# Kernel optimization log

Measured on AMD Instinct MI355X. Metric: run time of the kernel, lower is better.

Reference implementation:

```python
import jax, jax.numpy as jnp
import numpy as np
from math import pi

FC_IN, FC_OUT = 64, 64
LABEL_NC = 35
B, C, H, W = 2, 64, 128, 128
EPS = 1e-5
SLOPE = 0.01  # torch leaky_relu default


def _pa(h, w):
    # absolute normalized coordinates, matches init_pos buffers
    xs = (jnp.arange(h, dtype=jnp.float32) / h) * 2.0 - 1.0
    ys = (jnp.arange(w, dtype=jnp.float32) / w) * 2.0 - 1.0
    px = jnp.broadcast_to(xs[:, None], (h, w))
    py = jnp.broadcast_to(ys[None, :], (h, w))
    return jnp.stack([px, py], 0)  # (2,h,w)


def _coords(h, w):
    # f0=3; while-loop runs once (f=3 -> f=1), so exactly 4 channels
    f = 3.0
    ang_x = 2.0 * pi * jnp.remainder(jnp.arange(w, dtype=jnp.float32), f) / f
    ang_y = 2.0 * pi * jnp.remainder(jnp.arange(h, dtype=jnp.float32), f) / f
    xcos = jnp.broadcast_to(jnp.cos(ang_x)[None, :], (h, w))
    xsin = jnp.broadcast_to(jnp.sin(ang_x)[None, :], (h, w))
    ycos = jnp.broadcast_to(jnp.cos(ang_y)[:, None], (h, w))
    ysin = jnp.broadcast_to(jnp.sin(ang_y)[:, None], (h, w))
    return jnp.stack([xcos, xsin, ycos, ysin], 0)  # (4,h,w)


def _nearest(t, h, w):
    # F.interpolate(mode='nearest') index map: floor(i*in/out)
    ih = jnp.arange(h) * t.shape[2] // h
    iw = jnp.arange(w) * t.shape[3] // w
    return t[:, :, ih][:, :, :, iw]


def setup_inputs() -> dict:
    key = jax.random.key(0)
    ks = jax.random.split(key, 7)
    return {
        "x": jax.random.normal(ks[0], (B, C, H, W), jnp.float32),
        "layout": jax.random.normal(ks[1], (B, LABEL_NC, H, W), jnp.float32),
        "pr": jax.random.normal(ks[2], (B, 2, H, W), jnp.float32),
        "conv_w": jax.random.normal(ks[3], (1, 10), jnp.float32) * 0.02,
        "conv_b": jnp.zeros((1,), jnp.float32),
        "W_table": jax.random.normal(ks[4], (LABEL_NC, FC_IN * FC_OUT), jnp.float32),
        "b_table": jax.random.normal(ks[5], (LABEL_NC, FC_OUT), jnp.float32) * 0.02,
        "pl": jax.random.normal(ks[6], (2, H, W), jnp.float32),
    }


def reference(x, layout, pr, conv_w, conv_b, W_table, b_table, pl):
    b, c, h, w = x.shape
    pa = jnp.broadcast_to(_pa(h, w)[None], (b, 2, h, w))
    plb = jnp.broadcast_to(pl[None], (b, 2, h, w))
    coords = jnp.broadcast_to(_coords(h, w)[None], (b, 4, h, w))
    prr = _nearest(pr, h, w)
    pos = jnp.concatenate([pa, plb, prr, coords], axis=1)  # (B,10,h,w)
    # 1x1 conv to a single channel, broadcast-added over C
    x = x + jnp.einsum('bchw,oc->bohw', pos, conv_w) + conv_b[None, :, None, None]
    # argmax-routed per-pixel affine params
    lay = _nearest(layout, h, w)
    arg = jnp.argmax(lay, axis=1)  # (B,h,w) int
    Wg = W_table[arg].reshape(b, h, w, FC_IN, FC_OUT)  # huge gathered tensor (as in original)
    bg = b_table[arg]  # (B,h,w,FC_OUT)
    xh = jnp.transpose(x, (0, 2, 3, 1))  # (B,h,w,C)
    y = jnp.einsum('bhwc,bhwco->bhwo', xh, Wg) + bg
    y = jnp.transpose(y, (0, 3, 1, 2))  # (B,FC_OUT,h,w)
    # instance norm (no affine, biased variance, eps=1e-5)
    mu = jnp.mean(y, axis=(2, 3), keepdims=True)
    var = jnp.var(y, axis=(2, 3), keepdims=True)
    y = (y - mu) * jax.lax.rsqrt(var + EPS)
    return jnp.where(y >= 0, y, SLOPE * y)
```

## Files before the change

kernel.cpp:

```cpp
#include <hip/hip_runtime.h>

#define HH 128
#define WW 128
#define CC 64
#define OO 64
#define NC 35
#define NPIX (HH*WW)
#define LISTST NPIX
#define NBKT (2*NC)
#define XSTR 68


__global__ __launch_bounds__(256) void prep_kernel(
    const float* __restrict__ x, const float* __restrict__ layout,
    const float* __restrict__ pr, const float* __restrict__ cw,
    const float* __restrict__ cb, const float* __restrict__ pl,
    float* __restrict__ xT, int* __restrict__ lab)
{
    __shared__ float s_xh[64*33];
    __shared__ float s_s[32];

    const int t    = threadIdx.x;
    const int wv   = t >> 6;
    const int lane = t & 63;
    const int tile = blockIdx.x;
    const int b    = tile >> 9;
    const int rem  = tile & 511;
    const int h    = rem >> 2;
    const int w0   = (rem & 3) << 5;

    if (wv == 0 && lane < 32) {
        int w = w0 + lane;
        float pxv = (float)h * (2.0f/128.0f) - 1.0f;
        float pyv = (float)w * (2.0f/128.0f) - 1.0f;
        float pl0 = pl[h*WW + w];
        float pl1 = pl[NPIX + h*WW + w];
        float pr0 = pr[((b*2+0)*HH + h)*WW + w];
        float pr1 = pr[((b*2+1)*HH + h)*WW + w];
        int kx = w % 3, kyy = h % 3;
        const float C1 = -0.5f, S1 = 0.86602540378443864676f;
        float xcv = (kx==0)  ? 1.0f : C1;
        float xsv = (kx==0)  ? 0.0f : ((kx==1)  ? S1 : -S1);
        float ycv = (kyy==0) ? 1.0f : C1;
        float ysv = (kyy==0) ? 0.0f : ((kyy==1) ? S1 : -S1);
        s_s[lane] = cb[0] + pxv*cw[0] + pyv*cw[1] + pl0*cw[2] + pl1*cw[3]
                  + pr0*cw[4] + pr1*cw[5] + xcv*cw[6] + xsv*cw[7]
                  + ycv*cw[8] + ysv*cw[9];
    }

    if (wv == 1 && lane < 32) {
        int w = w0 + lane;
        const float* lp = layout + ((size_t)(b*NC)*HH + h)*WW + w;
        float best = lp[0]; int bi = 0;
        #pragma unroll
        for (int c = 1; c < NC; ++c) {
            float v = lp[(size_t)c*NPIX];
            if (v > best) { best = v; bi = c; }
        }
        lab[b*NPIX + h*WW + w] = bi;
    }

    {
        int p = t & 31, c0 = t >> 5;
        const float* xp = x + ((size_t)(b*CC)*HH + h)*WW + w0 + p;
        #pragma unroll
        for (int k = 0; k < 8; ++k) {
            int c = c0 + 8*k;
            s_xh[c*33 + p] = xp[(size_t)c*NPIX];
        }
    }
    __syncthreads();

    {
        int p = t >> 3, c0 = (t & 7) << 3;
        float sp = s_s[p];
        float4 a, d;
        a.x = s_xh[(c0+0)*33+p] + sp;
        a.y = s_xh[(c0+1)*33+p] + sp;
        a.z = s_xh[(c0+2)*33+p] + sp;
        a.w = s_xh[(c0+3)*33+p] + sp;
        d.x = s_xh[(c0+4)*33+p] + sp;
        d.y = s_xh[(c0+5)*33+p] + sp;
        d.z = s_xh[(c0+6)*33+p] + sp;
        d.w = s_xh[(c0+7)*33+p] + sp;
        float* dst = xT + (((size_t)b*NPIX + h*WW + w0 + p) << 6) + c0;
        *(float4*)dst       = a;
        *(float4*)(dst + 4) = d;
    }
}

__global__ __launch_bounds__(256) void bin_kernel(
    const int* __restrict__ lab, int* __restrict__ cnt, int* __restrict__ list)
{
    __shared__ int s_wsum[4];
    const int t    = threadIdx.x;
    const int lane = t & 63;
    const int wv   = t >> 6;
    const int bkt  = blockIdx.x;
    const int b    = (bkt >= NC) ? 1 : 0;
    const int l    = bkt - b*NC;
    const int* lp  = lab + b*NPIX;

    int m = 0;
    #pragma unroll 8
    for (int j = 0; j < 64; ++j) m += (lp[j*256 + t] == l) ? 1 : 0;

    int v = m;
    #pragma unroll
    for (int d = 1; d < 64; d <<= 1) {
        int o = __shfl_up(v, d);
        if (lane >= d) v += o;
    }
    if (lane == 63) s_wsum[wv] = v;
    __syncthreads();
    int wbase = 0;
    #pragma unroll
    for (int k = 0; k < 4; ++k) wbase += (k < wv) ? s_wsum[k] : 0;
    int base = wbase + v - m;
    if (t == 0) cnt[bkt] = s_wsum[0] + s_wsum[1] + s_wsum[2] + s_wsum[3];

    int* dst = list + bkt*LISTST;
    int o = base;
    #pragma unroll 8
    for (int j = 0; j < 64; ++j) {
        int p = j*256 + t;
        if (lp[p] == l) dst[o++] = p;
    }
}

#define FMA_PX(A, XV) \
    A.x = fmaf((XV), qv.x, A.x); \
    A.y = fmaf((XV), qv.y, A.y); \
    A.z = fmaf((XV), qv.z, A.z); \
    A.w = fmaf((XV), qv.w, A.w);

__global__ __launch_bounds__(256) void mv_kernel(
    const float* __restrict__ Wt, const float* __restrict__ bt,
    const float* __restrict__ xT, const int* __restrict__ cnt,
    const int* __restrict__ list, float* __restrict__ yT,
    float* __restrict__ gpad)
{
    __shared__ __align__(16) float s_xh[64*XSTR];
    __shared__ int   s_pib[64];
    __shared__ float s_red[4][64][2];
    __shared__ int   s_ntask;

    const int t    = threadIdx.x;
    const int wv   = t >> 6;
    const int lane = t & 63;
    const int i15  = lane & 15;
    const int ihi  = lane >> 4;

    if (t < 64) {
        int c1 = cnt[(lane < NBKT) ? lane : (NBKT-1)];
        int c2 = cnt[(lane < (NBKT-64)) ? 64 + lane : (NBKT-1)];
        int m  = c1 > c2 ? c1 : c2;
        #pragma unroll
        for (int d = 32; d >= 1; d >>= 1) {
            int o = __shfl_xor(m, d);
            m = m > o ? m : o;
        }
        if (lane == 0) s_ntask = NBKT * ((m + 63) >> 6);
    }
    __syncthreads();
    const int ntask = s_ntask;

    for (int task = blockIdx.x; task < ntask; task += gridDim.x) {
        const int bkt   = task % NBKT;
        const int chunk = task / NBKT;
        const int n     = cnt[bkt];
        const int base  = chunk << 6;
        if (base >= n) continue;
        const int b = (bkt >= NC) ? 1 : 0;
        const int l = bkt - b*NC;

        __syncthreads();

        {
            const int p   = t & 63;
            const int q   = t >> 6;
            const int pi  = base + p;
            const int pib = list[bkt*LISTST + ((pi < n) ? pi : (n-1))];
            if (q == 0) s_pib[p] = pib;
            const float* xp = xT + (((size_t)b*NPIX + pib) << 6) + (q << 4);
            #pragma unroll
            for (int j = 0; j < 4; ++j) {
                float4 v = ((const float4*)xp)[j];
                const int c = (q << 4) + (j << 2);
                s_xh[(c+0)*XSTR + p] = v.x;
                s_xh[(c+1)*XSTR + p] = v.y;
                s_xh[(c+2)*XSTR + p] = v.z;
                s_xh[(c+3)*XSTR + p] = v.w;
            }
        }
        __syncthreads();

        const float4* __restrict__ W4 = ((const float4*)(Wt + (size_t)l*4096)) + lane;
        const float4 bb = *((const float4*)(bt + (size_t)l*64) + i15);
        float4 sumv = make_float4(0,0,0,0), ssv = make_float4(0,0,0,0);

        #pragma unroll
        for (int g = 0; g < 2; ++g) {
            const int p0 = (wv << 4) + (g << 3);
            float4 a[8];
            #pragma unroll
            for (int pj = 0; pj < 8; ++pj) a[pj] = make_float4(0,0,0,0);

            #pragma unroll
            for (int tt = 0; tt < 16; ++tt) {
                const float4 qv = W4[tt << 6];
                const int    c  = (tt << 2) + ihi;
                const float4 xa = *(const float4*)&s_xh[c*XSTR + p0];
                const float4 xb = *(const float4*)&s_xh[c*XSTR + p0 + 4];
                FMA_PX(a[0], xa.x) FMA_PX(a[1], xa.y) FMA_PX(a[2], xa.z) FMA_PX(a[3], xa.w)
                FMA_PX(a[4], xb.x) FMA_PX(a[5], xb.y) FMA_PX(a[6], xb.z) FMA_PX(a[7], xb.w)
            }

            #pragma unroll
            for (int pj = 0; pj < 8; ++pj) {
                a[pj].x += __shfl_xor(a[pj].x, 16); a[pj].y += __shfl_xor(a[pj].y, 16);
                a[pj].z += __shfl_xor(a[pj].z, 16); a[pj].w += __shfl_xor(a[pj].w, 16);
                a[pj].x += __shfl_xor(a[pj].x, 32); a[pj].y += __shfl_xor(a[pj].y, 32);
                a[pj].z += __shfl_xor(a[pj].z, 32); a[pj].w += __shfl_xor(a[pj].w, 32);
            }

            if (ihi == 0) {
                #pragma unroll
                for (int pj = 0; pj < 8; ++pj) {
                    const bool  vld = (base + p0 + pj) < n;
                    const float msk = vld ? 1.0f : 0.0f;
                    float y0 = (a[pj].x + bb.x) * msk;
                    float y1 = (a[pj].y + bb.y) * msk;
                    float y2 = (a[pj].z + bb.z) * msk;
                    float y3 = (a[pj].w + bb.w) * msk;
                    if (vld) {
                        float* yp = yT + (((size_t)b*NPIX + s_pib[p0+pj]) << 6) + (i15 << 2);
                        *(float4*)yp = make_float4(y0, y1, y2, y3);
                    }
                    sumv.x += y0; ssv.x += y0*y0;
                    sumv.y += y1; ssv.y += y1*y1;
                    sumv.z += y2; ssv.z += y2*y2;
                    sumv.w += y3; ssv.w += y3*y3;
                }
            }
        }

        if (ihi == 0) {
            const int o = i15 << 2;
            s_red[wv][o+0][0] = sumv.x; s_red[wv][o+0][1] = ssv.x;
            s_red[wv][o+1][0] = sumv.y; s_red[wv][o+1][1] = ssv.y;
            s_red[wv][o+2][0] = sumv.z; s_red[wv][o+2][1] = ssv.z;
            s_red[wv][o+3][0] = sumv.w; s_red[wv][o+3][1] = ssv.w;
        }
        __syncthreads();
        if (t < 64) {
            float S  = s_red[0][t][0] + s_red[1][t][0] + s_red[2][t][0] + s_red[3][t][0];
            float SS = s_red[0][t][1] + s_red[1][t][1] + s_red[2][t][1] + s_red[3][t][1];
            float* gp = gpad + (((b << 6) + t) << 4);
            atomicAdd(gp + 0, S);
            atomicAdd(gp + 1, SS);
        }
    }
}

__global__ __launch_bounds__(256) void norm_kernel(
    const float* __restrict__ yT, const float* __restrict__ gpad,
    float* __restrict__ out)
{
    __shared__ float s_t[64*65];
    __shared__ float s_mean[64];
    __shared__ float s_rstd[64];

    const int t    = threadIdx.x;
    const int tile = blockIdx.x;
    const int b    = tile >> 8;
    const int rem  = tile & 255;
    const int h    = rem >> 1;
    const int w0   = (rem & 1) << 6;

    if (t < 64) {
        const float invN = 1.0f/16384.0f;
        const float* gp = gpad + (((b << 6) + t) << 4);
        float mean = gp[0] * invN;
        float var  = gp[1] * invN - mean*mean;
        s_mean[t] = mean;
        s_rstd[t] = rsqrtf(var + 1e-5f);
    }
    {
        const int p = t >> 2, q = t & 3;
        const float4* yp = (const float4*)(yT + (((size_t)b*NPIX + h*WW + w0 + p) << 6) + (q << 4));
        #pragma unroll
        for (int j = 0; j < 4; ++j) {
            float4 v = yp[j];
            int o = (q << 4) + (j << 2);
            s_t[(o+0)*65 + p] = v.x;
            s_t[(o+1)*65 + p] = v.y;
            s_t[(o+2)*65 + p] = v.z;
            s_t[(o+3)*65 + p] = v.w;
        }
    }
    __syncthreads();
    {
        const int o = t >> 2, q = t & 3;
        const float mean = s_mean[o];
        const float r    = s_rstd[o];
        float* op = out + (((size_t)(b*OO + o)*HH + h)*WW) + w0 + (q << 4);
        #pragma unroll
        for (int j = 0; j < 4; ++j) {
            int wq = (q << 4) + (j << 2);
            float4 v;
            v.x = s_t[o*65 + wq + 0];
            v.y = s_t[o*65 + wq + 1];
            v.z = s_t[o*65 + wq + 2];
            v.w = s_t[o*65 + wq + 3];
            float a_;
            a_ = (v.x - mean) * r; v.x = (a_ >= 0.f) ? a_ : 0.01f*a_;
            a_ = (v.y - mean) * r; v.y = (a_ >= 0.f) ? a_ : 0.01f*a_;
            a_ = (v.z - mean) * r; v.z = (a_ >= 0.f) ? a_ : 0.01f*a_;
            a_ = (v.w - mean) * r; v.w = (a_ >= 0.f) ? a_ : 0.01f*a_;
            ((float4*)op)[j] = v;
        }
    }
}

extern "C" void kernel_launch(void* const* d_in, const int* in_sizes, int n_in,
                              void* d_out, int out_size, void* d_ws, size_t ws_size,
                              hipStream_t stream) {
    const float* x      = (const float*)d_in[0];
    const float* layout = (const float*)d_in[1];
    const float* pr     = (const float*)d_in[2];
    const float* cw     = (const float*)d_in[3];
    const float* cb     = (const float*)d_in[4];
    const float* Wt     = (const float*)d_in[5];
    const float* bt     = (const float*)d_in[6];
    const float* pl     = (const float*)d_in[7];
    float* out = (float*)d_out;

    char*  ws   = (char*)d_ws;
    float* gpad = (float*)ws;
    int*   cnt  = (int*)(ws + 8192);
    int*   lab  = (int*)(ws + 16384);
    int*   list = (int*)(ws + (256u << 10));
    float* xT   = (float*)(ws + (8u  << 20));
    float* yT   = (float*)(ws + (16u << 20));

    hipMemsetAsync(gpad, 0, 8192, stream);
    prep_kernel<<<1024, 256, 0, stream>>>(x, layout, pr, cw, cb, pl, xT, lab);
    bin_kernel <<<  70, 256, 0, stream>>>(lab, cnt, list);
    mv_kernel  <<<1024, 256, 0, stream>>>(Wt, bt, xT, cnt, list, yT, gpad);
    norm_kernel<<< 512, 256, 0, stream>>>(yT, gpad, out);
}
```

Baseline: 128.1 us.

## Fuse all four stages into one cooperative persistent kernel with grid syncs

Replaces the memset plus four separate launches with a single cooperative kernel of 512 blocks that runs prep, binning, the routed matvec and the normalisation phases, separated by grid-wide syncs. Shared memory is unioned across phases, and the gpad zeroing moves into the binning phase. The aim is to remove launch gaps and kernel boundaries. In exchange, grid syncs are costly, each block does two prep tiles serially, and the binning phase runs on only 70 blocks while the rest wait. If the cooperative launch fails, the original multi-kernel path still runs.

```diff
diff --git a/kernel.cpp b/kernel.cpp
--- a/kernel.cpp
+++ b/kernel.cpp
@@ -1,4 +1,7 @@
 #include <hip/hip_runtime.h>
+#include <hip/hip_cooperative_groups.h>
+
+namespace cg = cooperative_groups;
 
 #define HH 128
 #define WW 128
@@ -9,6 +12,311 @@
 #define LISTST NPIX
 #define NBKT (2*NC)
 #define XSTR 68
+#define GRID 512
+
+
+#define FMA_PX(A, XV) \
+    A.x = fmaf((XV), qv.x, A.x); \
+    A.y = fmaf((XV), qv.y, A.y); \
+    A.z = fmaf((XV), qv.z, A.z); \
+    A.w = fmaf((XV), qv.w, A.w);
+
+__global__ void __launch_bounds__(256, 2) fused_kernel(
+    const float* __restrict__ x, const float* __restrict__ layout,
+    const float* __restrict__ pr, const float* __restrict__ cw,
+    const float* __restrict__ cb, const float* __restrict__ Wt,
+    const float* __restrict__ bt, const float* __restrict__ pl,
+    float* __restrict__ out, float* __restrict__ gpad, int* __restrict__ cnt,
+    int* __restrict__ lab, int* __restrict__ list,
+    float* __restrict__ xT, float* __restrict__ yT)
+{
+    __shared__ __align__(16) union {
+        struct { float xh[64*33]; float s[32]; } prep;
+        struct { int wsum[4]; } bin;
+        struct { float xh[64*XSTR]; float red[4][64][2]; int pib[64]; int ntask; } mv;
+        struct { float tmat[64*65]; float mean[64]; float rstd[64]; } norm;
+    } u;
+
+    cg::grid_group gg = cg::this_grid();
+
+    const int t    = threadIdx.x;
+    const int bid  = blockIdx.x;
+    const int wv   = t >> 6;
+    const int lane = t & 63;
+    const int i15  = lane & 15;
+    const int ihi  = lane >> 4;
+
+    for (int tile = bid; tile < 1024; tile += GRID) {
+        const int b  = tile >> 9;
+        const int rem = tile & 511;
+        const int h  = rem >> 2;
+        const int w0 = (rem & 3) << 5;
+
+        if (wv == 0 && lane < 32) {
+            int w = w0 + lane;
+            float pxv = (float)h * (2.0f/128.0f) - 1.0f;
+            float pyv = (float)w * (2.0f/128.0f) - 1.0f;
+            float pl0 = pl[h*WW + w];
+            float pl1 = pl[NPIX + h*WW + w];
+            float pr0 = pr[((b*2+0)*HH + h)*WW + w];
+            float pr1 = pr[((b*2+1)*HH + h)*WW + w];
+            int kx = w % 3, kyy = h % 3;
+            const float C1 = -0.5f, S1 = 0.86602540378443864676f;
+            float xcv = (kx==0)  ? 1.0f : C1;
+            float xsv = (kx==0)  ? 0.0f : ((kx==1)  ? S1 : -S1);
+            float ycv = (kyy==0) ? 1.0f : C1;
+            float ysv = (kyy==0) ? 0.0f : ((kyy==1) ? S1 : -S1);
+            u.prep.s[lane] = cb[0] + pxv*cw[0] + pyv*cw[1] + pl0*cw[2] + pl1*cw[3]
+                      + pr0*cw[4] + pr1*cw[5] + xcv*cw[6] + xsv*cw[7]
+                      + ycv*cw[8] + ysv*cw[9];
+        }
+
+        if (wv == 1 && lane < 32) {
+            int w = w0 + lane;
+            const float* lp = layout + ((size_t)(b*NC)*HH + h)*WW + w;
+            float best = lp[0]; int bi = 0;
+            #pragma unroll
+            for (int c = 1; c < NC; ++c) {
+                float v = lp[(size_t)c*NPIX];
+                if (v > best) { best = v; bi = c; }
+            }
+            lab[b*NPIX + h*WW + w] = bi;
+        }
+
+        {
+            int p = t & 31, c0 = t >> 5;
+            const float* xp = x + ((size_t)(b*CC)*HH + h)*WW + w0 + p;
+            #pragma unroll
+            for (int k = 0; k < 8; ++k) {
+                int c = c0 + 8*k;
+                u.prep.xh[c*33 + p] = xp[(size_t)c*NPIX];
+            }
+        }
+        __syncthreads();
+
+        {
+            int p = t >> 3, c0 = (t & 7) << 3;
+            float sp = u.prep.s[p];
+            float4 a, d;
+            a.x = u.prep.xh[(c0+0)*33+p] + sp;
+            a.y = u.prep.xh[(c0+1)*33+p] + sp;
+            a.z = u.prep.xh[(c0+2)*33+p] + sp;
+            a.w = u.prep.xh[(c0+3)*33+p] + sp;
+            d.x = u.prep.xh[(c0+4)*33+p] + sp;
+            d.y = u.prep.xh[(c0+5)*33+p] + sp;
+            d.z = u.prep.xh[(c0+6)*33+p] + sp;
+            d.w = u.prep.xh[(c0+7)*33+p] + sp;
+            float* dst = xT + (((size_t)b*NPIX + h*WW + w0 + p) << 6) + c0;
+            *(float4*)dst       = a;
+            *(float4*)(dst + 4) = d;
+        }
+        __syncthreads();
+    }
+
+    gg.sync();
+
+    if (bid < NBKT) {
+        const int bkt = bid;
+        const int b   = (bkt >= NC) ? 1 : 0;
+        const int l   = bkt - b*NC;
+        const int* lp = lab + b*NPIX;
+
+        int m = 0;
+        #pragma unroll 8
+        for (int j = 0; j < 64; ++j) m += (lp[j*256 + t] == l) ? 1 : 0;
+
+        int v = m;
+        #pragma unroll
+        for (int d = 1; d < 64; d <<= 1) {
+            int o = __shfl_up(v, d);
+            if (lane >= d) v += o;
+        }
+        if (lane == 63) u.bin.wsum[wv] = v;
+        __syncthreads();
+        int wbase = 0;
+        #pragma unroll
+        for (int k = 0; k < 4; ++k) wbase += (k < wv) ? u.bin.wsum[k] : 0;
+        int base = wbase + v - m;
+        if (t == 0) cnt[bkt] = u.bin.wsum[0] + u.bin.wsum[1] + u.bin.wsum[2] + u.bin.wsum[3];
+
+        int* dst = list + bkt*LISTST;
+        int o = base;
+        #pragma unroll 8
+        for (int j = 0; j < 64; ++j) {
+            int p = j*256 + t;
+            if (lp[p] == l) dst[o++] = p;
+        }
+    } else if (bid == NBKT) {
+        for (int i = t; i < 2048; i += 256) gpad[i] = 0.0f;
+    }
+
+    gg.sync();
+
+    if (t < 64) {
+        int c1 = cnt[(lane < NBKT) ? lane : (NBKT-1)];
+        int c2 = cnt[(lane < (NBKT-64)) ? 64 + lane : (NBKT-1)];
+        int m  = c1 > c2 ? c1 : c2;
+        #pragma unroll
+        for (int d = 32; d >= 1; d >>= 1) {
+            int o = __shfl_xor(m, d);
+            m = m > o ? m : o;
+        }
+        if (lane == 0) u.mv.ntask = NBKT * ((m + 63) >> 6);
+    }
+    __syncthreads();
+    const int ntask = u.mv.ntask;
+
+    for (int task = bid; task < ntask; task += GRID) {
+        const int bkt   = task % NBKT;
+        const int chunk = task / NBKT;
+        const int n     = cnt[bkt];
+        const int base  = chunk << 6;
+        if (base >= n) continue;
+        const int b = (bkt >= NC) ? 1 : 0;
+        const int l = bkt - b*NC;
+
+        __syncthreads();
+
+        {
+            const int p   = t & 63;
+            const int q   = t >> 6;
+            const int pi  = base + p;
+            const int pib = list[bkt*LISTST + ((pi < n) ? pi : (n-1))];
+            if (q == 0) u.mv.pib[p] = pib;
+            const float* xp = xT + (((size_t)b*NPIX + pib) << 6) + (q << 4);
+            #pragma unroll
+            for (int j = 0; j < 4; ++j) {
+                float4 v = ((const float4*)xp)[j];
+                const int c = (q << 4) + (j << 2);
+                u.mv.xh[(c+0)*XSTR + p] = v.x;
+                u.mv.xh[(c+1)*XSTR + p] = v.y;
+                u.mv.xh[(c+2)*XSTR + p] = v.z;
+                u.mv.xh[(c+3)*XSTR + p] = v.w;
+            }
+        }
+        __syncthreads();
+
+        const float4* __restrict__ W4 = ((const float4*)(Wt + (size_t)l*4096)) + lane;
+        const float4 bb = *((const float4*)(bt + (size_t)l*64) + i15);
+        float4 sumv = make_float4(0,0,0,0), ssv = make_float4(0,0,0,0);
+
+        #pragma unroll
+        for (int g = 0; g < 2; ++g) {
+            const int p0 = (wv << 4) + (g << 3);
+            float4 a[8];
+            #pragma unroll
+            for (int pj = 0; pj < 8; ++pj) a[pj] = make_float4(0,0,0,0);
+
+            #pragma unroll
+            for (int tt = 0; tt < 16; ++tt) {
+                const float4 qv = W4[tt << 6];
+                const int    c  = (tt << 2) + ihi;
+                const float4 xa = *(const float4*)&u.mv.xh[c*XSTR + p0];
+                const float4 xb = *(const float4*)&u.mv.xh[c*XSTR + p0 + 4];
+                FMA_PX(a[0], xa.x) FMA_PX(a[1], xa.y) FMA_PX(a[2], xa.z) FMA_PX(a[3], xa.w)
+                FMA_PX(a[4], xb.x) FMA_PX(a[5], xb.y) FMA_PX(a[6], xb.z) FMA_PX(a[7], xb.w)
+            }
+
+            #pragma unroll
+            for (int pj = 0; pj < 8; ++pj) {
+                a[pj].x += __shfl_xor(a[pj].x, 16); a[pj].y += __shfl_xor(a[pj].y, 16);
+                a[pj].z += __shfl_xor(a[pj].z, 16); a[pj].w += __shfl_xor(a[pj].w, 16);
+                a[pj].x += __shfl_xor(a[pj].x, 32); a[pj].y += __shfl_xor(a[pj].y, 32);
+                a[pj].z += __shfl_xor(a[pj].z, 32); a[pj].w += __shfl_xor(a[pj].w, 32);
+            }
+
+            if (ihi == 0) {
+                #pragma unroll
+                for (int pj = 0; pj < 8; ++pj) {
+                    const bool  vld = (base + p0 + pj) < n;
+                    const float msk = vld ? 1.0f : 0.0f;
+                    float y0 = (a[pj].x + bb.x) * msk;
+                    float y1 = (a[pj].y + bb.y) * msk;
+                    float y2 = (a[pj].z + bb.z) * msk;
+                    float y3 = (a[pj].w + bb.w) * msk;
+                    if (vld) {
+                        float* yp = yT + (((size_t)b*NPIX + u.mv.pib[p0+pj]) << 6) + (i15 << 2);
+                        *(float4*)yp = make_float4(y0, y1, y2, y3);
+                    }
+                    sumv.x += y0; ssv.x += y0*y0;
+                    sumv.y += y1; ssv.y += y1*y1;
+                    sumv.z += y2; ssv.z += y2*y2;
+                    sumv.w += y3; ssv.w += y3*y3;
+                }
+            }
+        }
+
+        if (ihi == 0) {
+            const int o = i15 << 2;
+            u.mv.red[wv][o+0][0] = sumv.x; u.mv.red[wv][o+0][1] = ssv.x;
+            u.mv.red[wv][o+1][0] = sumv.y; u.mv.red[wv][o+1][1] = ssv.y;
+            u.mv.red[wv][o+2][0] = sumv.z; u.mv.red[wv][o+2][1] = ssv.z;
+            u.mv.red[wv][o+3][0] = sumv.w; u.mv.red[wv][o+3][1] = ssv.w;
+        }
+        __syncthreads();
+        if (t < 64) {
+            float S  = u.mv.red[0][t][0] + u.mv.red[1][t][0] + u.mv.red[2][t][0] + u.mv.red[3][t][0];
+            float SS = u.mv.red[0][t][1] + u.mv.red[1][t][1] + u.mv.red[2][t][1] + u.mv.red[3][t][1];
+            float* gp = gpad + (((b << 6) + t) << 4);
+            atomicAdd(gp + 0, S);
+            atomicAdd(gp + 1, SS);
+        }
+    }
+
+    gg.sync();
+
+    {
+        const int tile = bid;
+        const int b    = tile >> 8;
+        const int rem  = tile & 255;
+        const int h    = rem >> 1;
+        const int w0   = (rem & 1) << 6;
+
+        if (t < 64) {
+            const float invN = 1.0f/16384.0f;
+            const float* gp = gpad + (((b << 6) + t) << 4);
+            float mean = gp[0] * invN;
+            float var  = gp[1] * invN - mean*mean;
+            u.norm.mean[t] = mean;
+            u.norm.rstd[t] = rsqrtf(var + 1e-5f);
+        }
+        {
+            const int p = t >> 2, q = t & 3;
+            const float4* yp = (const float4*)(yT + (((size_t)b*NPIX + h*WW + w0 + p) << 6) + (q << 4));
+            #pragma unroll
+            for (int j = 0; j < 4; ++j) {
+                float4 v = yp[j];
+                int o = (q << 4) + (j << 2);
+                u.norm.tmat[(o+0)*65 + p] = v.x;
+                u.norm.tmat[(o+1)*65 + p] = v.y;
+                u.norm.tmat[(o+2)*65 + p] = v.z;
+                u.norm.tmat[(o+3)*65 + p] = v.w;
+            }
+        }
+        __syncthreads();
+        {
+            const int o = t >> 2, q = t & 3;
+            const float mean = u.norm.mean[o];
+            const float r    = u.norm.rstd[o];
+            float* op = out + (((size_t)(b*OO + o)*HH + h)*WW) + w0 + (q << 4);
+            #pragma unroll
+            for (int j = 0; j < 4; ++j) {
+                int wq = (q << 4) + (j << 2);
+                float4 v;
+                v.x = u.norm.tmat[o*65 + wq + 0];
+                v.y = u.norm.tmat[o*65 + wq + 1];
+                v.z = u.norm.tmat[o*65 + wq + 2];
+                v.w = u.norm.tmat[o*65 + wq + 3];
+                float a_;
+                a_ = (v.x - mean) * r; v.x = (a_ >= 0.f) ? a_ : 0.01f*a_;
+                a_ = (v.y - mean) * r; v.y = (a_ >= 0.f) ? a_ : 0.01f*a_;
+                a_ = (v.z - mean) * r; v.z = (a_ >= 0.f) ? a_ : 0.01f*a_;
+                a_ = (v.w - mean) * r; v.w = (a_ >= 0.f) ? a_ : 0.01f*a_;
+                ((float4*)op)[j] = v;
+            }
+        }
+    }
+}
 
 
 __global__ __launch_bounds__(256) void prep_kernel(
@@ -19,15 +327,9 @@
 {
     __shared__ float s_xh[64*33];
     __shared__ float s_s[32];
-
-    const int t    = threadIdx.x;
-    const int wv   = t >> 6;
-    const int lane = t & 63;
-    const int tile = blockIdx.x;
-    const int b    = tile >> 9;
-    const int rem  = tile & 511;
-    const int h    = rem >> 2;
-    const int w0   = (rem & 3) << 5;
+    const int t = threadIdx.x, wv = t >> 6, lane = t & 63;
+    const int tile = blockIdx.x, b = tile >> 9, rem = tile & 511;
+    const int h = rem >> 2, w0 = (rem & 3) << 5;
 
     if (wv == 0 && lane < 32) {
         int w = w0 + lane;
@@ -47,7 +349,6 @@
                   + pr0*cw[4] + pr1*cw[5] + xcv*cw[6] + xsv*cw[7]
                   + ycv*cw[8] + ysv*cw[9];
     }
-
     if (wv == 1 && lane < 32) {
         int w = w0 + lane;
         const float* lp = layout + ((size_t)(b*NC)*HH + h)*WW + w;
@@ -59,33 +360,23 @@
         }
         lab[b*NPIX + h*WW + w] = bi;
     }
-
     {
         int p = t & 31, c0 = t >> 5;
         const float* xp = x + ((size_t)(b*CC)*HH + h)*WW + w0 + p;
         #pragma unroll
-        for (int k = 0; k < 8; ++k) {
-            int c = c0 + 8*k;
-            s_xh[c*33 + p] = xp[(size_t)c*NPIX];
-        }
+        for (int k = 0; k < 8; ++k) { int c = c0 + 8*k; s_xh[c*33 + p] = xp[(size_t)c*NPIX]; }
     }
     __syncthreads();
-
     {
         int p = t >> 3, c0 = (t & 7) << 3;
         float sp = s_s[p];
         float4 a, d;
-        a.x = s_xh[(c0+0)*33+p] + sp;
-        a.y = s_xh[(c0+1)*33+p] + sp;
-        a.z = s_xh[(c0+2)*33+p] + sp;
-        a.w = s_xh[(c0+3)*33+p] + sp;
-        d.x = s_xh[(c0+4)*33+p] + sp;
-        d.y = s_xh[(c0+5)*33+p] + sp;
-        d.z = s_xh[(c0+6)*33+p] + sp;
-        d.w = s_xh[(c0+7)*33+p] + sp;
+        a.x = s_xh[(c0+0)*33+p] + sp; a.y = s_xh[(c0+1)*33+p] + sp;
+        a.z = s_xh[(c0+2)*33+p] + sp; a.w = s_xh[(c0+3)*33+p] + sp;
+        d.x = s_xh[(c0+4)*33+p] + sp; d.y = s_xh[(c0+5)*33+p] + sp;
+        d.z = s_xh[(c0+6)*33+p] + sp; d.w = s_xh[(c0+7)*33+p] + sp;
         float* dst = xT + (((size_t)b*NPIX + h*WW + w0 + p) << 6) + c0;
-        *(float4*)dst       = a;
-        *(float4*)(dst + 4) = d;
+        *(float4*)dst = a; *(float4*)(dst + 4) = d;
     }
 }
 
@@ -93,24 +384,15 @@
     const int* __restrict__ lab, int* __restrict__ cnt, int* __restrict__ list)
 {
     __shared__ int s_wsum[4];
-    const int t    = threadIdx.x;
-    const int lane = t & 63;
-    const int wv   = t >> 6;
-    const int bkt  = blockIdx.x;
-    const int b    = (bkt >= NC) ? 1 : 0;
-    const int l    = bkt - b*NC;
-    const int* lp  = lab + b*NPIX;
-
+    const int t = threadIdx.x, lane = t & 63, wv = t >> 6;
+    const int bkt = blockIdx.x, b = (bkt >= NC) ? 1 : 0, l = bkt - b*NC;
+    const int* lp = lab + b*NPIX;
     int m = 0;
     #pragma unroll 8
     for (int j = 0; j < 64; ++j) m += (lp[j*256 + t] == l) ? 1 : 0;
-
     int v = m;
     #pragma unroll
-    for (int d = 1; d < 64; d <<= 1) {
-        int o = __shfl_up(v, d);
-        if (lane >= d) v += o;
-    }
+    for (int d = 1; d < 64; d <<= 1) { int o = __shfl_up(v, d); if (lane >= d) v += o; }
     if (lane == 63) s_wsum[wv] = v;
     __syncthreads();
     int wbase = 0;
@@ -118,21 +400,11 @@
     for (int k = 0; k < 4; ++k) wbase += (k < wv) ? s_wsum[k] : 0;
     int base = wbase + v - m;
     if (t == 0) cnt[bkt] = s_wsum[0] + s_wsum[1] + s_wsum[2] + s_wsum[3];
-
     int* dst = list + bkt*LISTST;
     int o = base;
     #pragma unroll 8
-    for (int j = 0; j < 64; ++j) {
-        int p = j*256 + t;
-        if (lp[p] == l) dst[o++] = p;
-    }
+    for (int j = 0; j < 64; ++j) { int p = j*256 + t; if (lp[p] == l) dst[o++] = p; }
 }
-
-#define FMA_PX(A, XV) \
-    A.x = fmaf((XV), qv.x, A.x); \
-    A.y = fmaf((XV), qv.y, A.y); \
-    A.z = fmaf((XV), qv.z, A.z); \
-    A.w = fmaf((XV), qv.w, A.w);
 
 __global__ __launch_bounds__(256) void mv_kernel(
     const float* __restrict__ Wt, const float* __restrict__ bt,
@@ -144,42 +416,28 @@
     __shared__ int   s_pib[64];
     __shared__ float s_red[4][64][2];
     __shared__ int   s_ntask;
-
-    const int t    = threadIdx.x;
-    const int wv   = t >> 6;
-    const int lane = t & 63;
-    const int i15  = lane & 15;
-    const int ihi  = lane >> 4;
+    const int t = threadIdx.x, wv = t >> 6, lane = t & 63;
+    const int i15 = lane & 15, ihi = lane >> 4;
 
     if (t < 64) {
         int c1 = cnt[(lane < NBKT) ? lane : (NBKT-1)];
         int c2 = cnt[(lane < (NBKT-64)) ? 64 + lane : (NBKT-1)];
         int m  = c1 > c2 ? c1 : c2;
         #pragma unroll
-        for (int d = 32; d >= 1; d >>= 1) {
-            int o = __shfl_xor(m, d);
-            m = m > o ? m : o;
-        }
+        for (int d = 32; d >= 1; d >>= 1) { int o = __shfl_xor(m, d); m = m > o ? m : o; }
         if (lane == 0) s_ntask = NBKT * ((m + 63) >> 6);
     }
     __syncthreads();
     const int ntask = s_ntask;
 
     for (int task = blockIdx.x; task < ntask; task += gridDim.x) {
-        const int bkt   = task % NBKT;
-        const int chunk = task / NBKT;
-        const int n     = cnt[bkt];
-        const int base  = chunk << 6;
+        const int bkt = task % NBKT, chunk = task / NBKT;
+        const int n = cnt[bkt], base = chunk << 6;
         if (base >= n) continue;
-        const int b = (bkt >= NC) ? 1 : 0;
-        const int l = bkt - b*NC;
-
-        __syncthreads();
-
+        const int b = (bkt >= NC) ? 1 : 0, l = bkt - b*NC;
+        __syncthreads();
         {
-            const int p   = t & 63;
-            const int q   = t >> 6;
-            const int pi  = base + p;
+            const int p = t & 63, q = t >> 6, pi = base + p;
             const int pib = list[bkt*LISTST + ((pi < n) ? pi : (n-1))];
             if (q == 0) s_pib[p] = pib;
             const float* xp = xT + (((size_t)b*NPIX + pib) << 6) + (q << 4);
@@ -187,25 +445,20 @@
             for (int j = 0; j < 4; ++j) {
                 float4 v = ((const float4*)xp)[j];
                 const int c = (q << 4) + (j << 2);
-                s_xh[(c+0)*XSTR + p] = v.x;
-                s_xh[(c+1)*XSTR + p] = v.y;
-                s_xh[(c+2)*XSTR + p] = v.z;
-                s_xh[(c+3)*XSTR + p] = v.w;
-            }
-        }
-        __syncthreads();
-
+                s_xh[(c+0)*XSTR + p] = v.x; s_xh[(c+1)*XSTR + p] = v.y;
+                s_xh[(c+2)*XSTR + p] = v.z; s_xh[(c+3)*XSTR + p] = v.w;
+            }
+        }
+        __syncthreads();
         const float4* __restrict__ W4 = ((const float4*)(Wt + (size_t)l*4096)) + lane;
         const float4 bb = *((const float4*)(bt + (size_t)l*64) + i15);
         float4 sumv = make_float4(0,0,0,0), ssv = make_float4(0,0,0,0);
-
         #pragma unroll
         for (int g = 0; g < 2; ++g) {
             const int p0 = (wv << 4) + (g << 3);
             float4 a[8];
             #pragma unroll
             for (int pj = 0; pj < 8; ++pj) a[pj] = make_float4(0,0,0,0);
-
             #pragma unroll
             for (int tt = 0; tt < 16; ++tt) {
                 const float4 qv = W4[tt << 6];
@@ -215,7 +468,6 @@
                 FMA_PX(a[0], xa.x) FMA_PX(a[1], xa.y) FMA_PX(a[2], xa.z) FMA_PX(a[3], xa.w)
                 FMA_PX(a[4], xb.x) FMA_PX(a[5], xb.y) FMA_PX(a[6], xb.z) FMA_PX(a[7], xb.w)
             }
-
             #pragma unroll
             for (int pj = 0; pj < 8; ++pj) {
                 a[pj].x += __shfl_xor(a[pj].x, 16); a[pj].y += __shfl_xor(a[pj].y, 16);
@@ -223,7 +475,6 @@
                 a[pj].x += __shfl_xor(a[pj].x, 32); a[pj].y += __shfl_xor(a[pj].y, 32);
                 a[pj].z += __shfl_xor(a[pj].z, 32); a[pj].w += __shfl_xor(a[pj].w, 32);
             }
-
             if (ihi == 0) {
                 #pragma unroll
                 for (int pj = 0; pj < 8; ++pj) {
@@ -244,7 +495,6 @@
                 }
             }
         }
-
         if (ihi == 0) {
             const int o = i15 << 2;
             s_red[wv][o+0][0] = sumv.x; s_red[wv][o+0][1] = ssv.x;
@@ -270,14 +520,8 @@
     __shared__ float s_t[64*65];
     __shared__ float s_mean[64];
     __shared__ float s_rstd[64];
-
-    const int t    = threadIdx.x;
-    const int tile = blockIdx.x;
-    const int b    = tile >> 8;
-    const int rem  = tile & 255;
-    const int h    = rem >> 1;
-    const int w0   = (rem & 1) << 6;
-
+    const int t = threadIdx.x, tile = blockIdx.x;
+    const int b = tile >> 8, rem = tile & 255, h = rem >> 1, w0 = (rem & 1) << 6;
     if (t < 64) {
         const float invN = 1.0f/16384.0f;
         const float* gp = gpad + (((b << 6) + t) << 4);
@@ -293,26 +537,21 @@
         for (int j = 0; j < 4; ++j) {
             float4 v = yp[j];
             int o = (q << 4) + (j << 2);
-            s_t[(o+0)*65 + p] = v.x;
-            s_t[(o+1)*65 + p] = v.y;
-            s_t[(o+2)*65 + p] = v.z;
-            s_t[(o+3)*65 + p] = v.w;
+            s_t[(o+0)*65 + p] = v.x; s_t[(o+1)*65 + p] = v.y;
+            s_t[(o+2)*65 + p] = v.z; s_t[(o+3)*65 + p] = v.w;
         }
     }
     __syncthreads();
     {
         const int o = t >> 2, q = t & 3;
-        const float mean = s_mean[o];
-        const float r    = s_rstd[o];
+        const float mean = s_mean[o], r = s_rstd[o];
         float* op = out + (((size_t)(b*OO + o)*HH + h)*WW) + w0 + (q << 4);
         #pragma unroll
         for (int j = 0; j < 4; ++j) {
             int wq = (q << 4) + (j << 2);
             float4 v;
-            v.x = s_t[o*65 + wq + 0];
-            v.y = s_t[o*65 + wq + 1];
-            v.z = s_t[o*65 + wq + 2];
-            v.w = s_t[o*65 + wq + 3];
+            v.x = s_t[o*65 + wq + 0]; v.y = s_t[o*65 + wq + 1];
+            v.z = s_t[o*65 + wq + 2]; v.w = s_t[o*65 + wq + 3];
             float a_;
             a_ = (v.x - mean) * r; v.x = (a_ >= 0.f) ? a_ : 0.01f*a_;
             a_ = (v.y - mean) * r; v.y = (a_ >= 0.f) ? a_ : 0.01f*a_;
@@ -344,9 +583,19 @@
     float* xT   = (float*)(ws + (8u  << 20));
     float* yT   = (float*)(ws + (16u << 20));
 
-    hipMemsetAsync(gpad, 0, 8192, stream);
-    prep_kernel<<<1024, 256, 0, stream>>>(x, layout, pr, cw, cb, pl, xT, lab);
-    bin_kernel <<<  70, 256, 0, stream>>>(lab, cnt, list);
-    mv_kernel  <<<1024, 256, 0, stream>>>(Wt, bt, xT, cnt, list, yT, gpad);
-    norm_kernel<<< 512, 256, 0, stream>>>(yT, gpad, out);
+    void* kargs[] = {
+        (void*)&x, (void*)&layout, (void*)&pr, (void*)&cw, (void*)&cb,
+        (void*)&Wt, (void*)&bt, (void*)&pl, (void*)&out,
+        (void*)&gpad, (void*)&cnt, (void*)&lab, (void*)&list,
+        (void*)&xT, (void*)&yT
+    };
+    hipError_t e = hipLaunchCooperativeKernel((const void*)fused_kernel,
+                                              dim3(GRID), dim3(256), kargs, 0, stream);
+    if (e != hipSuccess) {
+        hipMemsetAsync(gpad, 0, 8192, stream);
+        prep_kernel<<<1024, 256, 0, stream>>>(x, layout, pr, cw, cb, pl, xT, lab);
+        bin_kernel <<<  70, 256, 0, stream>>>(lab, cnt, list);
+        mv_kernel  <<<1024, 256, 0, stream>>>(Wt, bt, xT, cnt, list, yT, gpad);
+        norm_kernel<<< 512, 256, 0, stream>>>(yT, gpad, out);
+    }
 }
```

After: 293.4 us. 2.29x slower.

## Halve mv task size, widen bin kernel, fold gpad zeroing into prep

Applied to the files above, without the earlier changes.

Pixel chunks per mv task shrink from 64 to 32, each warp now owns 8 pixels instead of two groups of 8, and the mv grid grows to 1536 blocks. Together these give more parallel tasks and less padding waste in small buckets. bin_kernel moves to 1024 threads per block so each thread loops fewer times. The separate memset of the stats buffer is replaced by zeroing inside prep_kernel, which saves one launch. The trade-off is that each W-table fetch is reused over fewer pixels, and there are more atomics per bucket.

```diff
diff --git a/kernel.cpp b/kernel.cpp
--- a/kernel.cpp
+++ b/kernel.cpp
@@ -8,14 +8,14 @@
 #define NPIX (HH*WW)
 #define LISTST NPIX
 #define NBKT (2*NC)
-#define XSTR 68
+#define MSTR 36
 
 
 __global__ __launch_bounds__(256) void prep_kernel(
     const float* __restrict__ x, const float* __restrict__ layout,
     const float* __restrict__ pr, const float* __restrict__ cw,
     const float* __restrict__ cb, const float* __restrict__ pl,
-    float* __restrict__ xT, int* __restrict__ lab)
+    float* __restrict__ xT, int* __restrict__ lab, float* __restrict__ gpad)
 {
     __shared__ float s_xh[64*33];
     __shared__ float s_s[32];
@@ -28,6 +28,8 @@
     const int rem  = tile & 511;
     const int h    = rem >> 2;
     const int w0   = (rem & 3) << 5;
+
+    if (tile < 8) gpad[(tile << 8) + t] = 0.0f;
 
     if (wv == 0 && lane < 32) {
         int w = w0 + lane;
@@ -89,21 +91,21 @@
     }
 }
 
-__global__ __launch_bounds__(256) void bin_kernel(
+__global__ __launch_bounds__(1024) void bin_kernel(
     const int* __restrict__ lab, int* __restrict__ cnt, int* __restrict__ list)
 {
-    __shared__ int s_wsum[4];
+    __shared__ int s_wsum[16];
     const int t    = threadIdx.x;
     const int lane = t & 63;
-    const int wv   = t >> 6;
+    const int wvv  = t >> 6;
     const int bkt  = blockIdx.x;
     const int b    = (bkt >= NC) ? 1 : 0;
     const int l    = bkt - b*NC;
     const int* lp  = lab + b*NPIX;
 
     int m = 0;
-    #pragma unroll 8
-    for (int j = 0; j < 64; ++j) m += (lp[j*256 + t] == l) ? 1 : 0;
+    #pragma unroll
+    for (int j = 0; j < 16; ++j) m += (lp[j*1024 + t] == l) ? 1 : 0;
 
     int v = m;
     #pragma unroll
@@ -111,19 +113,24 @@
         int o = __shfl_up(v, d);
         if (lane >= d) v += o;
     }
-    if (lane == 63) s_wsum[wv] = v;
+    if (lane == 63) s_wsum[wvv] = v;
     __syncthreads();
     int wbase = 0;
     #pragma unroll
-    for (int k = 0; k < 4; ++k) wbase += (k < wv) ? s_wsum[k] : 0;
+    for (int k = 0; k < 16; ++k) wbase += (k < wvv) ? s_wsum[k] : 0;
     int base = wbase + v - m;
-    if (t == 0) cnt[bkt] = s_wsum[0] + s_wsum[1] + s_wsum[2] + s_wsum[3];
+    if (t == 0) {
+        int s = 0;
+        #pragma unroll
+        for (int k = 0; k < 16; ++k) s += s_wsum[k];
+        cnt[bkt] = s;
+    }
 
     int* dst = list + bkt*LISTST;
     int o = base;
-    #pragma unroll 8
-    for (int j = 0; j < 64; ++j) {
-        int p = j*256 + t;
+    #pragma unroll
+    for (int j = 0; j < 16; ++j) {
+        int p = j*1024 + t;
         if (lp[p] == l) dst[o++] = p;
     }
 }
@@ -140,8 +147,8 @@
     const int* __restrict__ list, float* __restrict__ yT,
     float* __restrict__ gpad)
 {
-    __shared__ __align__(16) float s_xh[64*XSTR];
-    __shared__ int   s_pib[64];
+    __shared__ __align__(16) float s_xh[64*MSTR];
+    __shared__ int   s_pib[32];
     __shared__ float s_red[4][64][2];
     __shared__ int   s_ntask;
 
@@ -160,7 +167,7 @@
             int o = __shfl_xor(m, d);
             m = m > o ? m : o;
         }
-        if (lane == 0) s_ntask = NBKT * ((m + 63) >> 6);
+        if (lane == 0) s_ntask = NBKT * ((m + 31) >> 5);
     }
     __syncthreads();
     const int ntask = s_ntask;
@@ -169,7 +176,7 @@
         const int bkt   = task % NBKT;
         const int chunk = task / NBKT;
         const int n     = cnt[bkt];
-        const int base  = chunk << 6;
+        const int base  = chunk << 5;
         if (base >= n) continue;
         const int b = (bkt >= NC) ? 1 : 0;
         const int l = bkt - b*NC;
@@ -177,75 +184,71 @@
         __syncthreads();
 
         {
-            const int p   = t & 63;
-            const int q   = t >> 6;
+            const int p   = t & 31;
+            const int e   = t >> 5;
             const int pi  = base + p;
             const int pib = list[bkt*LISTST + ((pi < n) ? pi : (n-1))];
-            if (q == 0) s_pib[p] = pib;
-            const float* xp = xT + (((size_t)b*NPIX + pib) << 6) + (q << 4);
-            #pragma unroll
-            for (int j = 0; j < 4; ++j) {
-                float4 v = ((const float4*)xp)[j];
-                const int c = (q << 4) + (j << 2);
-                s_xh[(c+0)*XSTR + p] = v.x;
-                s_xh[(c+1)*XSTR + p] = v.y;
-                s_xh[(c+2)*XSTR + p] = v.z;
-                s_xh[(c+3)*XSTR + p] = v.w;
-            }
+            if (e == 0) s_pib[p] = pib;
+            const float* xp = xT + (((size_t)b*NPIX + pib) << 6) + (e << 3);
+            float4 v0 = ((const float4*)xp)[0];
+            float4 v1 = ((const float4*)xp)[1];
+            const int c = e << 3;
+            s_xh[(c+0)*MSTR + p] = v0.x;
+            s_xh[(c+1)*MSTR + p] = v0.y;
+            s_xh[(c+2)*MSTR + p] = v0.z;
+            s_xh[(c+3)*MSTR + p] = v0.w;
+            s_xh[(c+4)*MSTR + p] = v1.x;
+            s_xh[(c+5)*MSTR + p] = v1.y;
+            s_xh[(c+6)*MSTR + p] = v1.z;
+            s_xh[(c+7)*MSTR + p] = v1.w;
         }
         __syncthreads();
 
         const float4* __restrict__ W4 = ((const float4*)(Wt + (size_t)l*4096)) + lane;
         const float4 bb = *((const float4*)(bt + (size_t)l*64) + i15);
+        const int p0 = wv << 3;
+
+        float4 a[8];
+        #pragma unroll
+        for (int pj = 0; pj < 8; ++pj) a[pj] = make_float4(0,0,0,0);
+
+        #pragma unroll
+        for (int tt = 0; tt < 16; ++tt) {
+            const float4 qv = W4[tt << 6];
+            const int    c  = (tt << 2) + ihi;
+            const float4 xa = *(const float4*)&s_xh[c*MSTR + p0];
+            const float4 xb = *(const float4*)&s_xh[c*MSTR + p0 + 4];
+            FMA_PX(a[0], xa.x) FMA_PX(a[1], xa.y) FMA_PX(a[2], xa.z) FMA_PX(a[3], xa.w)
+            FMA_PX(a[4], xb.x) FMA_PX(a[5], xb.y) FMA_PX(a[6], xb.z) FMA_PX(a[7], xb.w)
+        }
+
+        #pragma unroll
+        for (int pj = 0; pj < 8; ++pj) {
+            a[pj].x += __shfl_xor(a[pj].x, 16); a[pj].y += __shfl_xor(a[pj].y, 16);
+            a[pj].z += __shfl_xor(a[pj].z, 16); a[pj].w += __shfl_xor(a[pj].w, 16);
+            a[pj].x += __shfl_xor(a[pj].x, 32); a[pj].y += __shfl_xor(a[pj].y, 32);
+            a[pj].z += __shfl_xor(a[pj].z, 32); a[pj].w += __shfl_xor(a[pj].w, 32);
+        }
+
         float4 sumv = make_float4(0,0,0,0), ssv = make_float4(0,0,0,0);
-
-        #pragma unroll
-        for (int g = 0; g < 2; ++g) {
-            const int p0 = (wv << 4) + (g << 3);
-            float4 a[8];
-            #pragma unroll
-            for (int pj = 0; pj < 8; ++pj) a[pj] = make_float4(0,0,0,0);
-
-            #pragma unroll
-            for (int tt = 0; tt < 16; ++tt) {
-                const float4 qv = W4[tt << 6];
-                const int    c  = (tt << 2) + ihi;
-                const float4 xa = *(const float4*)&s_xh[c*XSTR + p0];
-                const float4 xb = *(const float4*)&s_xh[c*XSTR + p0 + 4];
-                FMA_PX(a[0], xa.x) FMA_PX(a[1], xa.y) FMA_PX(a[2], xa.z) FMA_PX(a[3], xa.w)
-                FMA_PX(a[4], xb.x) FMA_PX(a[5], xb.y) FMA_PX(a[6], xb.z) FMA_PX(a[7], xb.w)
-            }
-
+        if (ihi == 0) {
             #pragma unroll
             for (int pj = 0; pj < 8; ++pj) {
-                a[pj].x += __shfl_xor(a[pj].x, 16); a[pj].y += __shfl_xor(a[pj].y, 16);
-                a[pj].z += __shfl_xor(a[pj].z, 16); a[pj].w += __shfl_xor(a[pj].w, 16);
-                a[pj].x += __shfl_xor(a[pj].x, 32); a[pj].y += __shfl_xor(a[pj].y, 32);
-                a[pj].z += __shfl_xor(a[pj].z, 32); a[pj].w += __shfl_xor(a[pj].w, 32);
+                const bool  vld = (base + p0 + pj) < n;
+                const float msk = vld ? 1.0f : 0.0f;
+                float y0 = (a[pj].x + bb.x) * msk;
+                float y1 = (a[pj].y + bb.y) * msk;
+                float y2 = (a[pj].z + bb.z) * msk;
+                float y3 = (a[pj].w + bb.w) * msk;
+                if (vld) {
+                    float* yp = yT + (((size_t)b*NPIX + s_pib[p0+pj]) << 6) + (i15 << 2);
+                    *(float4*)yp = make_float4(y0, y1, y2, y3);
+                }
+                sumv.x += y0; ssv.x += y0*y0;
+                sumv.y += y1; ssv.y += y1*y1;
+                sumv.z += y2; ssv.z += y2*y2;
+                sumv.w += y3; ssv.w += y3*y3;
             }
-
-            if (ihi == 0) {
-                #pragma unroll
-                for (int pj = 0; pj < 8; ++pj) {
-                    const bool  vld = (base + p0 + pj) < n;
-                    const float msk = vld ? 1.0f : 0.0f;
-                    float y0 = (a[pj].x + bb.x) * msk;
-                    float y1 = (a[pj].y + bb.y) * msk;
-                    float y2 = (a[pj].z + bb.z) * msk;
-                    float y3 = (a[pj].w + bb.w) * msk;
-                    if (vld) {
-                        float* yp = yT + (((size_t)b*NPIX + s_pib[p0+pj]) << 6) + (i15 << 2);
-                        *(float4*)yp = make_float4(y0, y1, y2, y3);
-                    }
-                    sumv.x += y0; ssv.x += y0*y0;
-                    sumv.y += y1; ssv.y += y1*y1;
-                    sumv.z += y2; ssv.z += y2*y2;
-                    sumv.w += y3; ssv.w += y3*y3;
-                }
-            }
-        }
-
-        if (ihi == 0) {
             const int o = i15 << 2;
             s_red[wv][o+0][0] = sumv.x; s_red[wv][o+0][1] = ssv.x;
             s_red[wv][o+1][0] = sumv.y; s_red[wv][o+1][1] = ssv.y;
@@ -344,9 +347,8 @@
     float* xT   = (float*)(ws + (8u  << 20));
     float* yT   = (float*)(ws + (16u << 20));
 
-    hipMemsetAsync(gpad, 0, 8192, stream);
-    prep_kernel<<<1024, 256, 0, stream>>>(x, layout, pr, cw, cb, pl, xT, lab);
-    bin_kernel <<<  70, 256, 0, stream>>>(lab, cnt, list);
-    mv_kernel  <<<1024, 256, 0, stream>>>(Wt, bt, xT, cnt, list, yT, gpad);
-    norm_kernel<<< 512, 256, 0, stream>>>(yT, gpad, out);
-}
+    prep_kernel<<<1024,  256, 0, stream>>>(x, layout, pr, cw, cb, pl, xT, lab, gpad);
+    bin_kernel <<<  70, 1024, 0, stream>>>(lab, cnt, list);
+    mv_kernel  <<<1536,  256, 0, stream>>>(Wt, bt, xT, cnt, list, yT, gpad);
+    norm_kernel<<< 512,  256, 0, stream>>>(yT, gpad, out);
+}
```

Result: no change. 128.2 us (+0.1%).

## Replace atomic stat accumulation with per-task partials and a stats reduction kernel

Applied to the files above, without the earlier changes.

Instead of atomically adding per-task channel sums into a memset buffer, the matvec kernel writes per-task partial sums to a strided buffer, and a new stats kernel reduces them into mean and rstd per (batch, channel). This removes the memset launch and atomic contention, and makes the reduction deterministic. The bin kernel is also widened to 1024 threads with fewer loop iterations. The cost is an extra kernel launch and extra partial-sum traffic.

```diff
diff --git a/kernel.cpp b/kernel.cpp
--- a/kernel.cpp
+++ b/kernel.cpp
@@ -9,6 +9,7 @@
 #define LISTST NPIX
 #define NBKT (2*NC)
 #define XSTR 68
+#define TST  17920
 
 
 __global__ __launch_bounds__(256) void prep_kernel(
@@ -89,21 +90,21 @@
     }
 }
 
-__global__ __launch_bounds__(256) void bin_kernel(
+__global__ __launch_bounds__(1024) void bin_kernel(
     const int* __restrict__ lab, int* __restrict__ cnt, int* __restrict__ list)
 {
-    __shared__ int s_wsum[4];
+    __shared__ int s_wsum[16];
     const int t    = threadIdx.x;
     const int lane = t & 63;
-    const int wv   = t >> 6;
+    const int wvv  = t >> 6;
     const int bkt  = blockIdx.x;
     const int b    = (bkt >= NC) ? 1 : 0;
     const int l    = bkt - b*NC;
     const int* lp  = lab + b*NPIX;
 
     int m = 0;
-    #pragma unroll 8
-    for (int j = 0; j < 64; ++j) m += (lp[j*256 + t] == l) ? 1 : 0;
+    #pragma unroll
+    for (int j = 0; j < 16; ++j) m += (lp[j*1024 + t] == l) ? 1 : 0;
 
     int v = m;
     #pragma unroll
@@ -111,19 +112,24 @@
         int o = __shfl_up(v, d);
         if (lane >= d) v += o;
     }
-    if (lane == 63) s_wsum[wv] = v;
+    if (lane == 63) s_wsum[wvv] = v;
     __syncthreads();
     int wbase = 0;
     #pragma unroll
-    for (int k = 0; k < 4; ++k) wbase += (k < wv) ? s_wsum[k] : 0;
+    for (int k = 0; k < 16; ++k) wbase += (k < wvv) ? s_wsum[k] : 0;
     int base = wbase + v - m;
-    if (t == 0) cnt[bkt] = s_wsum[0] + s_wsum[1] + s_wsum[2] + s_wsum[3];
+    if (t == 0) {
+        int s = 0;
+        #pragma unroll
+        for (int k = 0; k < 16; ++k) s += s_wsum[k];
+        cnt[bkt] = s;
+    }
 
     int* dst = list + bkt*LISTST;
     int o = base;
-    #pragma unroll 8
-    for (int j = 0; j < 64; ++j) {
-        int p = j*256 + t;
+    #pragma unroll
+    for (int j = 0; j < 16; ++j) {
+        int p = j*1024 + t;
         if (lp[p] == l) dst[o++] = p;
     }
 }
@@ -138,7 +144,7 @@
     const float* __restrict__ Wt, const float* __restrict__ bt,
     const float* __restrict__ xT, const int* __restrict__ cnt,
     const int* __restrict__ list, float* __restrict__ yT,
-    float* __restrict__ gpad)
+    float* __restrict__ psum, float* __restrict__ pss)
 {
     __shared__ __align__(16) float s_xh[64*XSTR];
     __shared__ int   s_pib[64];
@@ -170,7 +176,13 @@
         const int chunk = task / NBKT;
         const int n     = cnt[bkt];
         const int base  = chunk << 6;
-        if (base >= n) continue;
+        if (base >= n) {
+            if (t < 64) {
+                psum[(size_t)t*TST + task] = 0.0f;
+                pss [(size_t)t*TST + task] = 0.0f;
+            }
+            continue;
+        }
         const int b = (bkt >= NC) ? 1 : 0;
         const int l = bkt - b*NC;
 
@@ -256,15 +268,67 @@
         if (t < 64) {
             float S  = s_red[0][t][0] + s_red[1][t][0] + s_red[2][t][0] + s_red[3][t][0];
             float SS = s_red[0][t][1] + s_red[1][t][1] + s_red[2][t][1] + s_red[3][t][1];
-            float* gp = gpad + (((b << 6) + t) << 4);
-            atomicAdd(gp + 0, S);
-            atomicAdd(gp + 1, SS);
-        }
+            psum[(size_t)t*TST + task] = S;
+            pss [(size_t)t*TST + task] = SS;
+        }
+    }
+}
+
+__global__ __launch_bounds__(256) void stats_kernel(
+    const float* __restrict__ psum, const float* __restrict__ pss,
+    const int* __restrict__ cnt, float* __restrict__ stats)
+{
+    __shared__ float s_red[4][2];
+    __shared__ int   s_nt;
+    const int e    = blockIdx.x;
+    const int b    = e >> 6;
+    const int o    = e & 63;
+    const int t    = threadIdx.x;
+    const int lane = t & 63;
+    const int wv   = t >> 6;
+
+    if (t < 64) {
+        int c1 = cnt[(lane < NBKT) ? lane : (NBKT-1)];
+        int c2 = cnt[(lane < (NBKT-64)) ? 64 + lane : (NBKT-1)];
+        int m  = c1 > c2 ? c1 : c2;
+        #pragma unroll
+        for (int d = 32; d >= 1; d >>= 1) {
+            int x = __shfl_xor(m, d);
+            m = m > x ? m : x;
+        }
+        if (lane == 0) s_nt = NBKT * ((m + 63) >> 6);
+    }
+    __syncthreads();
+    const int ntask = s_nt;
+
+    float S = 0.0f, SS = 0.0f;
+    const float* pr_ = psum + (size_t)o*TST;
+    const float* pq_ = pss  + (size_t)o*TST;
+    for (int i = t; i < ntask; i += 256) {
+        int bkt = i % NBKT;
+        int bi  = (bkt >= NC) ? 1 : 0;
+        if (bi == b) { S += pr_[i]; SS += pq_[i]; }
+    }
+    #pragma unroll
+    for (int d = 32; d >= 1; d >>= 1) {
+        S += __shfl_xor(S, d);
+        SS += __shfl_xor(SS, d);
+    }
+    if (lane == 0) { s_red[wv][0] = S; s_red[wv][1] = SS; }
+    __syncthreads();
+    if (t == 0) {
+        float s  = s_red[0][0] + s_red[1][0] + s_red[2][0] + s_red[3][0];
+        float ss = s_red[0][1] + s_red[1][1] + s_red[2][1] + s_red[3][1];
+        const float invN = 1.0f/16384.0f;
+        float mean = s * invN;
+        float var  = ss * invN - mean*mean;
+        stats[e*2+0] = mean;
+        stats[e*2+1] = rsqrtf(var + 1e-5f);
     }
 }
 
 __global__ __launch_bounds__(256) void norm_kernel(
-    const float* __restrict__ yT, const float* __restrict__ gpad,
+    const float* __restrict__ yT, const float* __restrict__ stats,
     float* __restrict__ out)
 {
     __shared__ float s_t[64*65];
@@ -279,12 +343,9 @@
     const int w0   = (rem & 1) << 6;
 
     if (t < 64) {
-        const float invN = 1.0f/16384.0f;
-        const float* gp = gpad + (((b << 6) + t) << 4);
-        float mean = gp[0] * invN;
-        float var  = gp[1] * invN - mean*mean;
-        s_mean[t] = mean;
-        s_rstd[t] = rsqrtf(var + 1e-5f);
+        const int e = (b << 6) + t;
+        s_mean[t] = stats[e*2+0];
+        s_rstd[t] = stats[e*2+1];
     }
     {
         const int p = t >> 2, q = t & 3;
@@ -336,17 +397,19 @@
     const float* pl     = (const float*)d_in[7];
     float* out = (float*)d_out;
 
-    char*  ws   = (char*)d_ws;
-    float* gpad = (float*)ws;
-    int*   cnt  = (int*)(ws + 8192);
-    int*   lab  = (int*)(ws + 16384);
-    int*   list = (int*)(ws + (256u << 10));
-    float* xT   = (float*)(ws + (8u  << 20));
-    float* yT   = (float*)(ws + (16u << 20));
-
-    hipMemsetAsync(gpad, 0, 8192, stream);
-    prep_kernel<<<1024, 256, 0, stream>>>(x, layout, pr, cw, cb, pl, xT, lab);
-    bin_kernel <<<  70, 256, 0, stream>>>(lab, cnt, list);
-    mv_kernel  <<<1024, 256, 0, stream>>>(Wt, bt, xT, cnt, list, yT, gpad);
-    norm_kernel<<< 512, 256, 0, stream>>>(yT, gpad, out);
-}
+    char*  ws    = (char*)d_ws;
+    int*   cnt   = (int*)ws;
+    float* stats = (float*)(ws + 1024);
+    int*   lab   = (int*)(ws + 16384);
+    int*   list  = (int*)(ws + (256u << 10));
+    float* xT    = (float*)(ws + (8u  << 20));
+    float* yT    = (float*)(ws + (16u << 20));
+    float* psum  = (float*)(ws + (32u << 20));
+    float* pss   = (float*)(ws + (48u << 20));
+
+    prep_kernel <<<1024,  256, 0, stream>>>(x, layout, pr, cw, cb, pl, xT, lab);
+    bin_kernel  <<<  70, 1024, 0, stream>>>(lab, cnt, list);
+    mv_kernel   <<<1024,  256, 0, stream>>>(Wt, bt, xT, cnt, list, yT, psum, pss);
+    stats_kernel<<< 128,  256, 0, stream>>>(psum, pss, cnt, stats);
+    norm_kernel <<< 512,  256, 0, stream>>>(yT, stats, out);
+}
```

New measurement: 109.3 us. 1.17x faster.
